# Performance work log

Measured on AMD Instinct MI355X. Metric: run time of the kernel, lower is better.

The kernel has to match this reference:

```python
import jax, jax.numpy as jnp
import numpy as np

B, T, D = 8, 2048, 1024
NUM_HEADS = 16
SCALE = 1.0 / np.sqrt(D // NUM_HEADS).astype(np.float32)  # sqrt(d_modal//num_heads), per source


def setup_inputs() -> dict:
    key = jax.random.key(0)
    ks = jax.random.split(key, 7)
    s = 1.0 / np.sqrt(D).astype(np.float32)
    return {
        "x": jax.random.normal(ks[0], (B, T, D), dtype=jnp.float32),
        "Wq_w": jax.random.normal(ks[1], (D, D), dtype=jnp.float32) * s,
        "Wq_b": jax.random.normal(ks[2], (D,), dtype=jnp.float32) * 0.01,
        "Wk_w": jax.random.normal(ks[3], (D, D), dtype=jnp.float32) * s,
        "Wk_b": jax.random.normal(ks[4], (D,), dtype=jnp.float32) * 0.01,
        "Wv_w": jax.random.normal(ks[5], (D, D), dtype=jnp.float32) * s,
        "Wv_b": jax.random.normal(ks[6], (D,), dtype=jnp.float32) * 0.01,
    }


def reference(x, Wq_w, Wq_b, Wk_w, Wk_b, Wv_w, Wv_b):
    # Linear projections (torch nn.Linear: y = x @ W.T + b)
    Q = jnp.einsum('btd,ed->bte', x, Wq_w) + Wq_b
    K = jnp.einsum('btd,ed->bte', x, Wk_w) + Wk_b
    V = jnp.einsum('btd,ed->bte', x, Wv_w) + Wv_b
    # scores [B, T, T], scaled by 1/sqrt(d_modal // num_heads) as in source
    scores = jnp.einsum('bqd,bkd->bqk', Q, K) * SCALE
    causal = jnp.tril(jnp.ones((T, T), dtype=bool))  # tril mask buffer
    scores = jnp.where(causal, scores, -jnp.inf)
    attn = jax.nn.softmax(scores, axis=-1)
    return jnp.einsum('bqk,bkd->bqd', attn, V)
```

## Files before the change

kernel.cpp:

```cpp
#include <hip/hip_runtime.h>


typedef float f32x4 __attribute__((ext_vector_type(4)));
typedef _Float16 half8 __attribute__((ext_vector_type(8)));
typedef _Float16 half4 __attribute__((ext_vector_type(4)));

#define DEVINL __device__ __forceinline__
static constexpr float ATT_SCALE = 0.125f;

DEVINL void gload_lds16(const _Float16* g, _Float16* l) {
  __builtin_amdgcn_global_load_lds((const __attribute__((address_space(1))) void*)g,
                                   (__attribute__((address_space(3))) void*)l, 16, 0, 0);
}

#define SBAR() __builtin_amdgcn_sched_barrier(0)

template <int LDA, int LDB, class GA, class GB>
DEVINL void gemm_2ph(GA ga, GB gb, int NT, char* ldsb, int tid, f32x4 acc[8][4]) {
  const int l = tid & 63, w = tid >> 6;
  const int wm = w >> 2, wn = w & 3;
  const int lr = l & 15, lk = l >> 4;
  int srow[2], scol[2];
#pragma unroll
  for (int i = 0; i < 2; ++i) {
    const int P = i * 512 + w * 64 + l;
    srow[i] = P >> 3;
    scol[i] = (P & 7) ^ (srow[i] & 7);
  }
  const int ch0 = ((lk ^ (lr & 7)) << 4);
  const int ch1 = (((lk + 4) ^ (lr & 7)) << 4);
  const int abase = lr * 128;
  const int bbase = (wn >> 1) * 16384 + (wn & 1) * 8192 + lr * 128;

  auto STGA = [&](int t, int bufb) {
#pragma unroll
    for (int h = 0; h < 2; ++h) {
      const _Float16* g0 = ga(t, h);
      char* dst = ldsb + bufb * 65536 + h * 16384;
#pragma unroll
      for (int i = 0; i < 2; ++i)
        gload_lds16(g0 + (size_t)srow[i] * LDA + scol[i] * 8,
                    (_Float16*)(dst + i * 8192 + w * 1024));
    }
  };
  auto STGB = [&](int t, int bufb) {
#pragma unroll
    for (int h = 0; h < 2; ++h) {
      const _Float16* g0 = gb(t, h);
      char* dst = ldsb + bufb * 65536 + 32768 + h * 16384;
#pragma unroll
      for (int i = 0; i < 2; ++i)
        gload_lds16(g0 + (size_t)srow[i] * LDB + scol[i] * 8,
                    (_Float16*)(dst + i * 8192 + w * 1024));
    }
  };
  half8 aA[4][2], aB[4][2], bC[4][2];
  auto RDA = [&](int bufb, int ih, half8 d[4][2]) {
    const char* sA = ldsb + bufb * 65536 + wm * 16384 + ih * 8192;
#pragma unroll
    for (int i = 0; i < 4; ++i) {
      d[i][0] = *(const half8*)(sA + abase + i * 2048 + ch0);
      d[i][1] = *(const half8*)(sA + abase + i * 2048 + ch1);
    }
  };
  auto RDB8 = [&](int bufb) {
    const char* sB = ldsb + bufb * 65536 + 32768;
#pragma unroll
    for (int j = 0; j < 4; ++j) {
      bC[j][0] = *(const half8*)(sB + bbase + j * 2048 + ch0);
      bC[j][1] = *(const half8*)(sB + bbase + j * 2048 + ch1);
    }
  };

#define MMQ() _Pragma("unroll") for (int kk_ = 0; kk_ < 2; ++kk_) \
    _Pragma("unroll") for (int i_ = 0; i_ < 4; ++i_) \
    _Pragma("unroll") for (int j_ = 0; j_ < 4; ++j_) \
      acc[i_][j_] = __builtin_amdgcn_mfma_f32_16x16x32_f16( \
          aA[i_][kk_], bC[j_][kk_], acc[i_][j_], 0, 0, 0);
#define MMH(JO) _Pragma("unroll") for (int kk_ = 0; kk_ < 2; ++kk_) \
    _Pragma("unroll") for (int i_ = 0; i_ < 4; ++i_) \
    _Pragma("unroll") for (int jj_ = 0; jj_ < 2; ++jj_) \
      acc[4 + i_][(JO) + jj_] = __builtin_amdgcn_mfma_f32_16x16x32_f16( \
          aB[i_][kk_], bC[(JO) + jj_][kk_], acc[4 + i_][(JO) + jj_], 0, 0, 0);

  STGA(0, 0); STGB(0, 0); STGB(1, 1);
  asm volatile("s_waitcnt vmcnt(4)" ::: "memory");
  __builtin_amdgcn_s_barrier(); SBAR();
  RDA(0, 0, aA);

  for (int t = 0; t < NT; ++t) {
    const int bufb = t & 1, obuf = bufb ^ 1;
    RDB8(bufb);
    RDA(bufb, 1, aB);
    if (t + 1 < NT) STGA(t + 1, obuf);
    SBAR(); __builtin_amdgcn_s_barrier();
    __builtin_amdgcn_s_setprio(1);
    MMQ();
    __builtin_amdgcn_s_setprio(0); SBAR();
    if (t + 2 < NT) {
      STGB(t + 2, bufb);
      asm volatile("s_waitcnt vmcnt(4)" ::: "memory");
    } else {
      asm volatile("s_waitcnt vmcnt(0)" ::: "memory");
    }
    SBAR(); __builtin_amdgcn_s_barrier();
    __builtin_amdgcn_s_setprio(1);
    MMH(0);
    MMH(2);
    __builtin_amdgcn_s_setprio(0);
    if (t + 1 < NT) RDA(obuf, 0, aA);
    SBAR();
  }
#undef MMQ
#undef MMH
}

template <int LDA, int LDB, class GA, class GB>
DEVINL void gemm_n128(GA ga, GB gb, int NT, char* ldsb, int tid, f32x4 acc[4][4]) {
  const int l = tid & 63, w = tid >> 6;
  const int wm = w >> 1, wn = w & 1;
  const int lr = l & 15, lk = l >> 4;
  int srow[2], scol[2];
#pragma unroll
  for (int i = 0; i < 2; ++i) {
    const int P = i * 512 + w * 64 + l;
    srow[i] = P >> 3;
    scol[i] = (P & 7) ^ (srow[i] & 7);
  }
  const int ch0 = ((lk ^ (lr & 7)) << 4);
  const int ch1 = (((lk + 4) ^ (lr & 7)) << 4);
  const int abase = (wm >> 1) * 16384 + ((wm & 1) * 64 + lr) * 128;
  const int bbase = 32768 + (wn * 64 + lr) * 128;

  auto STG = [&](const _Float16* g0, int ld, int bufb, int slot) {
    char* dst = ldsb + bufb * 49152 + slot * 16384;
#pragma unroll
    for (int i = 0; i < 2; ++i)
      gload_lds16(g0 + (size_t)srow[i] * ld + scol[i] * 8,
                  (_Float16*)(dst + i * 8192 + w * 1024));
  };
  half8 a[4][2], bfr[4][2];
  auto RD = [&](int bufb) {
    const char* bb = ldsb + bufb * 49152;
#pragma unroll
    for (int i = 0; i < 4; ++i) {
      a[i][0] = *(const half8*)(bb + abase + i * 2048 + ch0);
      a[i][1] = *(const half8*)(bb + abase + i * 2048 + ch1);
    }
#pragma unroll
    for (int j = 0; j < 4; ++j) {
      bfr[j][0] = *(const half8*)(bb + bbase + j * 2048 + ch0);
      bfr[j][1] = *(const half8*)(bb + bbase + j * 2048 + ch1);
    }
  };

  STG(ga(0, 0), LDA, 0, 0); STG(ga(0, 1), LDA, 0, 1); STG(gb(0), LDB, 0, 2);
  STG(ga(1, 0), LDA, 1, 0); STG(ga(1, 1), LDA, 1, 1); STG(gb(1), LDB, 1, 2);
  asm volatile("s_waitcnt vmcnt(6)" ::: "memory");
  __builtin_amdgcn_s_barrier();

  for (int t = 0; t < NT; ++t) {
    const int bufb = t & 1;
    RD(bufb);
    SBAR();
    __builtin_amdgcn_s_barrier();
    asm volatile("s_waitcnt lgkmcnt(0)" ::: "memory");
    SBAR();
    __builtin_amdgcn_s_setprio(1);
#pragma unroll
    for (int i = 0; i < 4; ++i)
#pragma unroll
      for (int j = 0; j < 4; ++j)
        acc[i][j] = __builtin_amdgcn_mfma_f32_16x16x32_f16(a[i][0], bfr[j][0], acc[i][j], 0, 0, 0);
    __builtin_amdgcn_s_setprio(0);
    SBAR();
    __builtin_amdgcn_s_barrier();
    if (t + 2 < NT) {
      STG(ga(t + 2, 0), LDA, bufb, 0);
      STG(ga(t + 2, 1), LDA, bufb, 1);
      STG(gb(t + 2), LDB, bufb, 2);
      asm volatile("s_waitcnt vmcnt(6)" ::: "memory");
    } else if (t + 1 < NT) {
      asm volatile("s_waitcnt vmcnt(0)" ::: "memory");
    }
    SBAR();
    __builtin_amdgcn_s_barrier();
    __builtin_amdgcn_s_setprio(1);
#pragma unroll
    for (int i = 0; i < 4; ++i)
#pragma unroll
      for (int j = 0; j < 4; ++j)
        acc[i][j] = __builtin_amdgcn_mfma_f32_16x16x32_f16(a[i][1], bfr[j][1], acc[i][j], 0, 0, 0);
    __builtin_amdgcn_s_setprio(0);
    SBAR();
    __builtin_amdgcn_s_barrier();
  }
}

__global__ __launch_bounds__(256) void cvt_all(const float* __restrict__ x,
                                               const float* __restrict__ wq,
                                               const float* __restrict__ wk,
                                               const float* __restrict__ wv,
                                               _Float16* __restrict__ xh,
                                               _Float16* __restrict__ wqh,
                                               _Float16* __restrict__ wkh,
                                               _Float16* __restrict__ wvh) {
  const int n8 = 2490368;
  for (int i = blockIdx.x * 256 + threadIdx.x; i < n8; i += 2048 * 256) {
    const float* src; _Float16* dst; int off;
    if (i < 2097152)      { src = x;  dst = xh;  off = i; }
    else if (i < 2228224) { src = wq; dst = wqh; off = i - 2097152; }
    else if (i < 2359296) { src = wk; dst = wkh; off = i - 2228224; }
    else                  { src = wv; dst = wvh; off = i - 2359296; }
    const float4* p = (const float4*)src + (size_t)off * 2;
    float4 v0 = p[0], v1 = p[1];
    half8 h;
    h[0] = (_Float16)v0.x; h[1] = (_Float16)v0.y; h[2] = (_Float16)v0.z; h[3] = (_Float16)v0.w;
    h[4] = (_Float16)v1.x; h[5] = (_Float16)v1.y; h[6] = (_Float16)v1.z; h[7] = (_Float16)v1.w;
    *((half8*)dst + off) = h;
  }
}

__global__ __launch_bounds__(512) void gemm_qkv(
    const _Float16* __restrict__ xh, const _Float16* __restrict__ Wqh,
    const _Float16* __restrict__ Wkh, const _Float16* __restrict__ Wvh,
    const float* __restrict__ bq, const float* __restrict__ bk,
    const float* __restrict__ bv, _Float16* __restrict__ Qh,
    _Float16* __restrict__ Kh, _Float16* __restrict__ VT) {
  __shared__ _Float16 lds[65536];
  const int tid = threadIdx.x;
  const int bid = blockIdx.x;
  const int swz = (bid & 7) * 96 + (bid >> 3);
  const int mt = swz / 12, nt = swz % 12;
  const int sel = nt >> 2;
  const _Float16* Wsel = sel == 0 ? Wqh : (sel == 1 ? Wkh : Wvh);
  const float* bsel = sel == 0 ? bq : (sel == 1 ? bk : bv);
  const _Float16* Ab = xh + (size_t)mt * 256 * 1024;
  const _Float16* Bb = Wsel + (size_t)(nt & 3) * 256 * 1024;
  f32x4 acc[8][4] = {};
  auto ga = [&](int t, int h) { return Ab + (size_t)h * 128 * 1024 + t * 64; };
  auto gb = [&](int t, int h) { return Bb + (size_t)h * 128 * 1024 + t * 64; };
  gemm_2ph<1024, 1024>(ga, gb, 16, (char*)lds, tid, acc);
  const int l = tid & 63, w = tid >> 6;
  const int wm = w >> 2, wn = w & 3;
  const int lr = l & 15, lk = l >> 4;
  const int n0 = (nt & 3) * 256;
  __syncthreads();
#pragma unroll
  for (int ai = 0; ai < 8; ++ai) {
    const int rbase = wm * 128 + (ai >> 2) * 64 + (ai & 3) * 16 + lk * 4;
#pragma unroll
    for (int j = 0; j < 4; ++j) {
      const int col = wn * 64 + j * 16 + lr;
      const float bvv = bsel[n0 + col];
#pragma unroll
      for (int r = 0; r < 4; ++r) {
        const int row = rbase + r;
        const float v = acc[ai][j][r] + bvv;
        if (sel < 2)
          lds[row * 256 + ((col + (row >> 2) * 16) & 255)] = (_Float16)v;
        else
          lds[col * 256 + ((row + (col >> 2) * 16) & 255)] = (_Float16)v;
      }
    }
  }
  __syncthreads();
#pragma unroll
  for (int i = 0; i < 16; ++i) {
    const int c = i * 512 + tid;
    const int row = c >> 5, c8 = c & 31;
    half8 v = *(const half8*)&lds[row * 256 + ((c8 * 8 + (row >> 2) * 16) & 255)];
    if (sel < 2) {
      _Float16* Out = sel == 0 ? Qh : Kh;
      *(half8*)&Out[(size_t)(mt * 256 + row) * 1024 + n0 + c8 * 8] = v;
    } else {
      const int bb = mt >> 3, t0 = (mt & 7) * 256;
      *(half8*)&VT[((size_t)bb * 1024 + n0 + row) * 2048 + t0 + c8 * 8] = v;
    }
  }
}

__global__ __launch_bounds__(512) void gemm_qk(const _Float16* __restrict__ Qh,
                                               const _Float16* __restrict__ Kh,
                                               _Float16* __restrict__ Sc) {
  __shared__ _Float16 lds[49152];
  const int tid = threadIdx.x;
  const int j = blockIdx.x;
  const int b = j / 72, r = j % 72;
  int qt = 0, cum = 0;
  while (cum + (qt + 1) * 2 <= r) { cum += (qt + 1) * 2; ++qt; }
  const int jn = r - cum;
  const _Float16* Ab = Qh + ((size_t)b * 2048 + qt * 256) * 1024;
  const _Float16* Bb = Kh + ((size_t)b * 2048 + jn * 128) * 1024;
  f32x4 acc[4][4] = {};
  auto ga = [&](int t, int h) { return Ab + (size_t)h * 128 * 1024 + t * 64; };
  auto gb = [&](int t) { return Bb + t * 64; };
  gemm_n128<1024, 1024>(ga, gb, 16, (char*)lds, tid, acc);
  const int l = tid & 63, w = tid >> 6;
  const int wm = w >> 1, wn = w & 1;
  const int lr = l & 15, lk = l >> 4;
  _Float16* St = Sc + ((size_t)b * 36 + (size_t)(qt * (qt + 1) / 2) + (jn >> 1)) * 65536 +
                 (jn & 1) * 128;
  const _Float16 NINF = (_Float16)(-__builtin_inff());
#pragma unroll
  for (int i = 0; i < 4; ++i) {
#pragma unroll
    for (int jj = 0; jj < 4; ++jj) {
      const int col = wn * 64 + jj * 16 + lr;
      const int kg = jn * 128 + col;
#pragma unroll
      for (int rr = 0; rr < 4; ++rr) {
        const int row = wm * 64 + i * 16 + lk * 4 + rr;
        const int qg = qt * 256 + row;
        St[(size_t)row * 256 + col] =
            (kg <= qg) ? (_Float16)(acc[i][jj][rr] * ATT_SCALE) : NINF;
      }
    }
  }
}

__global__ __launch_bounds__(256) void softmax_p(const _Float16* __restrict__ Sc,
                                                 _Float16* __restrict__ Pc) {
  const int l = threadIdx.x & 63;
  const int gid = blockIdx.x * 4 + (threadIdx.x >> 6);
  const int b = gid >> 11, q = gid & 2047;
  const int qt = q >> 8, rq = q & 255;
  const int ntile = qt + 1;
  const size_t base = ((size_t)b * 36 + (size_t)(qt * (qt + 1) / 2)) * 65536 +
                      (size_t)rq * 256 + l * 4;
  float vx[32];
  float m = -__builtin_inff();
#pragma unroll
  for (int c = 0; c < 8; ++c) {
    float x0 = -__builtin_inff(), x1 = x0, x2 = x0, x3 = x0;
    if (c < ntile) {
      half4 t = *(const half4*)&Sc[base + (size_t)c * 65536];
      x0 = (float)t[0]; x1 = (float)t[1]; x2 = (float)t[2]; x3 = (float)t[3];
    }
    vx[4 * c] = x0; vx[4 * c + 1] = x1; vx[4 * c + 2] = x2; vx[4 * c + 3] = x3;
    m = fmaxf(m, fmaxf(fmaxf(x0, x1), fmaxf(x2, x3)));
  }
#pragma unroll
  for (int s = 1; s < 64; s <<= 1) m = fmaxf(m, __shfl_xor(m, s, 64));
  float sum = 0.f;
#pragma unroll
  for (int i = 0; i < 32; ++i) { vx[i] = __expf(vx[i] - m); sum += vx[i]; }
#pragma unroll
  for (int s = 1; s < 64; s <<= 1) sum += __shfl_xor(sum, s, 64);
  const float inv = 1.f / sum;
  _Float16* Pb = Pc + base;
#pragma unroll
  for (int c = 0; c < 8; ++c) {
    if (c < ntile) {
      half4 p;
      p[0] = (_Float16)(vx[4 * c] * inv);
      p[1] = (_Float16)(vx[4 * c + 1] * inv);
      p[2] = (_Float16)(vx[4 * c + 2] * inv);
      p[3] = (_Float16)(vx[4 * c + 3] * inv);
      *(half4*)&Pb[(size_t)c * 65536] = p;
    }
  }
}

__global__ __launch_bounds__(512) void gemm_pv(const _Float16* __restrict__ Pc,
                                               const _Float16* __restrict__ VT,
                                               float* __restrict__ O) {
  __shared__ _Float16 lds[49152];
  const int tid = threadIdx.x;
  const int j = blockIdx.x;
  const int qt = 7 - (j >> 6);
  const int dt = (j >> 3) & 7, b = j & 7;
  const _Float16* Pb = Pc + ((size_t)b * 36 + (size_t)(qt * (qt + 1) / 2)) * 65536;
  const _Float16* Vb = VT + ((size_t)b * 1024 + dt * 128) * 2048;
  f32x4 acc[4][4] = {};
  auto ga = [&](int t, int h) {
    return Pb + (size_t)(t >> 2) * 65536 + (size_t)h * 32768 + (t & 3) * 64;
  };
  auto gb = [&](int t) { return Vb + t * 64; };
  gemm_n128<256, 2048>(ga, gb, (qt + 1) * 4, (char*)lds, tid, acc);
  const int l = tid & 63, w = tid >> 6;
  const int wm = w >> 1, wn = w & 1;
  const int lr = l & 15, lk = l >> 4;
#pragma unroll
  for (int i = 0; i < 4; ++i) {
#pragma unroll
    for (int jj = 0; jj < 4; ++jj) {
      const int cg = dt * 128 + wn * 64 + jj * 16 + lr;
#pragma unroll
      for (int rr = 0; rr < 4; ++rr) {
        const int rg = qt * 256 + wm * 64 + i * 16 + lk * 4 + rr;
        O[((size_t)b * 2048 + rg) * 1024 + cg] = acc[i][jj][rr];
      }
    }
  }
}

extern "C" void kernel_launch(void* const* d_in, const int* in_sizes, int n_in,
                              void* d_out, int out_size, void* d_ws, size_t ws_size,
                              hipStream_t stream) {
  const float* x    = (const float*)d_in[0];
  const float* Wq_w = (const float*)d_in[1];
  const float* Wq_b = (const float*)d_in[2];
  const float* Wk_w = (const float*)d_in[3];
  const float* Wk_b = (const float*)d_in[4];
  const float* Wv_w = (const float*)d_in[5];
  const float* Wv_b = (const float*)d_in[6];
  float* out = (float*)d_out;
  char* ws = (char*)d_ws;
  _Float16* xh  = (_Float16*)(ws);
  _Float16* Wqh = (_Float16*)(ws + 33554432);
  _Float16* Wkh = (_Float16*)(ws + 35651584);
  _Float16* Wvh = (_Float16*)(ws + 37748736);
  _Float16* Sc  = (_Float16*)(ws);
  _Float16* Qh  = (_Float16*)(ws + 75497472);
  _Float16* Kh  = (_Float16*)(ws + 109051904);
  _Float16* Pc  = (_Float16*)(ws + 75497472);
  _Float16* VT  = (_Float16*)(ws + 142606336);

  cvt_all<<<2048, 256, 0, stream>>>(x, Wq_w, Wk_w, Wv_w, xh, Wqh, Wkh, Wvh);
  gemm_qkv<<<768, 512, 0, stream>>>(xh, Wqh, Wkh, Wvh, Wq_b, Wk_b, Wv_b, Qh, Kh, VT);
  gemm_qk<<<576, 512, 0, stream>>>(Qh, Kh, Sc);
  softmax_p<<<4096, 256, 0, stream>>>(Sc, Pc);
  gemm_pv<<<512, 512, 0, stream>>>(Pc, VT, out);
}
```

Before: 274.0 us.

## Unify GEMMs into 256-thread 256x128 tiles with K=32 steps and smaller LDS

```diff
diff --git a/kernel.cpp b/kernel.cpp
--- a/kernel.cpp
+++ b/kernel.cpp
@@ -16,182 +16,73 @@
 #define SBAR() __builtin_amdgcn_sched_barrier(0)
 
 template <int LDA, int LDB, class GA, class GB>
-DEVINL void gemm_2ph(GA ga, GB gb, int NT, char* ldsb, int tid, f32x4 acc[8][4]) {
-  const int l = tid & 63, w = tid >> 6;
-  const int wm = w >> 2, wn = w & 3;
-  const int lr = l & 15, lk = l >> 4;
-  int srow[2], scol[2];
-#pragma unroll
-  for (int i = 0; i < 2; ++i) {
-    const int P = i * 512 + w * 64 + l;
-    srow[i] = P >> 3;
-    scol[i] = (P & 7) ^ (srow[i] & 7);
-  }
-  const int ch0 = ((lk ^ (lr & 7)) << 4);
-  const int ch1 = (((lk + 4) ^ (lr & 7)) << 4);
-  const int abase = lr * 128;
-  const int bbase = (wn >> 1) * 16384 + (wn & 1) * 8192 + lr * 128;
-
-  auto STGA = [&](int t, int bufb) {
-#pragma unroll
-    for (int h = 0; h < 2; ++h) {
-      const _Float16* g0 = ga(t, h);
-      char* dst = ldsb + bufb * 65536 + h * 16384;
-#pragma unroll
-      for (int i = 0; i < 2; ++i)
-        gload_lds16(g0 + (size_t)srow[i] * LDA + scol[i] * 8,
-                    (_Float16*)(dst + i * 8192 + w * 1024));
-    }
-  };
-  auto STGB = [&](int t, int bufb) {
-#pragma unroll
-    for (int h = 0; h < 2; ++h) {
-      const _Float16* g0 = gb(t, h);
-      char* dst = ldsb + bufb * 65536 + 32768 + h * 16384;
-#pragma unroll
-      for (int i = 0; i < 2; ++i)
-        gload_lds16(g0 + (size_t)srow[i] * LDB + scol[i] * 8,
-                    (_Float16*)(dst + i * 8192 + w * 1024));
-    }
-  };
-  half8 aA[4][2], aB[4][2], bC[4][2];
-  auto RDA = [&](int bufb, int ih, half8 d[4][2]) {
-    const char* sA = ldsb + bufb * 65536 + wm * 16384 + ih * 8192;
-#pragma unroll
-    for (int i = 0; i < 4; ++i) {
-      d[i][0] = *(const half8*)(sA + abase + i * 2048 + ch0);
-      d[i][1] = *(const half8*)(sA + abase + i * 2048 + ch1);
-    }
-  };
-  auto RDB8 = [&](int bufb) {
-    const char* sB = ldsb + bufb * 65536 + 32768;
-#pragma unroll
-    for (int j = 0; j < 4; ++j) {
-      bC[j][0] = *(const half8*)(sB + bbase + j * 2048 + ch0);
-      bC[j][1] = *(const half8*)(sB + bbase + j * 2048 + ch1);
-    }
-  };
-
-#define MMQ() _Pragma("unroll") for (int kk_ = 0; kk_ < 2; ++kk_) \
-    _Pragma("unroll") for (int i_ = 0; i_ < 4; ++i_) \
-    _Pragma("unroll") for (int j_ = 0; j_ < 4; ++j_) \
-      acc[i_][j_] = __builtin_amdgcn_mfma_f32_16x16x32_f16( \
-          aA[i_][kk_], bC[j_][kk_], acc[i_][j_], 0, 0, 0);
-#define MMH(JO) _Pragma("unroll") for (int kk_ = 0; kk_ < 2; ++kk_) \
-    _Pragma("unroll") for (int i_ = 0; i_ < 4; ++i_) \
-    _Pragma("unroll") for (int jj_ = 0; jj_ < 2; ++jj_) \
-      acc[4 + i_][(JO) + jj_] = __builtin_amdgcn_mfma_f32_16x16x32_f16( \
-          aB[i_][kk_], bC[(JO) + jj_][kk_], acc[4 + i_][(JO) + jj_], 0, 0, 0);
-
-  STGA(0, 0); STGB(0, 0); STGB(1, 1);
-  asm volatile("s_waitcnt vmcnt(4)" ::: "memory");
-  __builtin_amdgcn_s_barrier(); SBAR();
-  RDA(0, 0, aA);
-
-  for (int t = 0; t < NT; ++t) {
-    const int bufb = t & 1, obuf = bufb ^ 1;
-    RDB8(bufb);
-    RDA(bufb, 1, aB);
-    if (t + 1 < NT) STGA(t + 1, obuf);
-    SBAR(); __builtin_amdgcn_s_barrier();
-    __builtin_amdgcn_s_setprio(1);
-    MMQ();
-    __builtin_amdgcn_s_setprio(0); SBAR();
-    if (t + 2 < NT) {
-      STGB(t + 2, bufb);
-      asm volatile("s_waitcnt vmcnt(4)" ::: "memory");
-    } else {
-      asm volatile("s_waitcnt vmcnt(0)" ::: "memory");
-    }
-    SBAR(); __builtin_amdgcn_s_barrier();
-    __builtin_amdgcn_s_setprio(1);
-    MMH(0);
-    MMH(2);
-    __builtin_amdgcn_s_setprio(0);
-    if (t + 1 < NT) RDA(obuf, 0, aA);
-    SBAR();
-  }
-#undef MMQ
-#undef MMH
-}
-
-template <int LDA, int LDB, class GA, class GB>
-DEVINL void gemm_n128(GA ga, GB gb, int NT, char* ldsb, int tid, f32x4 acc[4][4]) {
+DEVINL void gemm_mb(GA ga, GB gb, int NT, char* ldsb, int tid, f32x4 acc[8][4]) {
   const int l = tid & 63, w = tid >> 6;
   const int wm = w >> 1, wn = w & 1;
   const int lr = l & 15, lk = l >> 4;
-  int srow[2], scol[2];
+  int arow[4], acol[4], brow[2], bcol[2];
+#pragma unroll
+  for (int i = 0; i < 4; ++i) {
+    const int P = i * 256 + tid;
+    arow[i] = P >> 2;
+    acol[i] = (P & 3) ^ ((arow[i] >> 1) & 3);
+  }
 #pragma unroll
   for (int i = 0; i < 2; ++i) {
-    const int P = i * 512 + w * 64 + l;
-    srow[i] = P >> 3;
-    scol[i] = (P & 7) ^ (srow[i] & 7);
-  }
-  const int ch0 = ((lk ^ (lr & 7)) << 4);
-  const int ch1 = (((lk + 4) ^ (lr & 7)) << 4);
-  const int abase = (wm >> 1) * 16384 + ((wm & 1) * 64 + lr) * 128;
-  const int bbase = 32768 + (wn * 64 + lr) * 128;
-
-  auto STG = [&](const _Float16* g0, int ld, int bufb, int slot) {
-    char* dst = ldsb + bufb * 49152 + slot * 16384;
+    const int P = i * 256 + tid;
+    brow[i] = P >> 2;
+    bcol[i] = (P & 3) ^ ((brow[i] >> 1) & 3);
+  }
+  int aoff[8], boff[4];
+#pragma unroll
+  for (int i = 0; i < 8; ++i) {
+    const int r = wm * 128 + i * 16 + lr;
+    aoff[i] = r * 64 + ((lk ^ ((r >> 1) & 3)) << 4);
+  }
+#pragma unroll
+  for (int j = 0; j < 4; ++j) {
+    const int r = wn * 64 + j * 16 + lr;
+    boff[j] = 16384 + r * 64 + ((lk ^ ((r >> 1) & 3)) << 4);
+  }
+  auto STG = [&](int t, int bufoff) {
+    const _Float16* gA = ga(t);
+#pragma unroll
+    for (int i = 0; i < 4; ++i)
+      gload_lds16(gA + (size_t)arow[i] * LDA + acol[i] * 8,
+                  (_Float16*)(ldsb + bufoff + i * 4096 + w * 1024));
+    const _Float16* gB = gb(t);
 #pragma unroll
     for (int i = 0; i < 2; ++i)
-      gload_lds16(g0 + (size_t)srow[i] * ld + scol[i] * 8,
-                  (_Float16*)(dst + i * 8192 + w * 1024));
+      gload_lds16(gB + (size_t)brow[i] * LDB + bcol[i] * 8,
+                  (_Float16*)(ldsb + bufoff + 16384 + i * 4096 + w * 1024));
   };
-  half8 a[4][2], bfr[4][2];
-  auto RD = [&](int bufb) {
-    const char* bb = ldsb + bufb * 49152;
-#pragma unroll
-    for (int i = 0; i < 4; ++i) {
-      a[i][0] = *(const half8*)(bb + abase + i * 2048 + ch0);
-      a[i][1] = *(const half8*)(bb + abase + i * 2048 + ch1);
-    }
-#pragma unroll
-    for (int j = 0; j < 4; ++j) {
-      bfr[j][0] = *(const half8*)(bb + bbase + j * 2048 + ch0);
-      bfr[j][1] = *(const half8*)(bb + bbase + j * 2048 + ch1);
-    }
-  };
-
-  STG(ga(0, 0), LDA, 0, 0); STG(ga(0, 1), LDA, 0, 1); STG(gb(0), LDB, 0, 2);
-  STG(ga(1, 0), LDA, 1, 0); STG(ga(1, 1), LDA, 1, 1); STG(gb(1), LDB, 1, 2);
+
+  STG(0, 0);
+  STG(1, 24576);
   asm volatile("s_waitcnt vmcnt(6)" ::: "memory");
   __builtin_amdgcn_s_barrier();
 
+  half8 a[8], b[4];
   for (int t = 0; t < NT; ++t) {
-    const int bufb = t & 1;
-    RD(bufb);
+    const int bufoff = (t & 1) * 24576;
+    const char* bb = ldsb + bufoff;
+#pragma unroll
+    for (int i = 0; i < 8; ++i) a[i] = *(const half8*)(bb + aoff[i]);
+#pragma unroll
+    for (int j = 0; j < 4; ++j) b[j] = *(const half8*)(bb + boff[j]);
+    asm volatile("s_waitcnt lgkmcnt(0)" ::: "memory");
     SBAR();
     __builtin_amdgcn_s_barrier();
-    asm volatile("s_waitcnt lgkmcnt(0)" ::: "memory");
-    SBAR();
+    if (t + 2 < NT) STG(t + 2, bufoff);
     __builtin_amdgcn_s_setprio(1);
 #pragma unroll
-    for (int i = 0; i < 4; ++i)
+    for (int i = 0; i < 8; ++i)
 #pragma unroll
       for (int j = 0; j < 4; ++j)
-        acc[i][j] = __builtin_amdgcn_mfma_f32_16x16x32_f16(a[i][0], bfr[j][0], acc[i][j], 0, 0, 0);
+        acc[i][j] = __builtin_amdgcn_mfma_f32_16x16x32_f16(a[i], b[j], acc[i][j], 0, 0, 0);
     __builtin_amdgcn_s_setprio(0);
-    SBAR();
-    __builtin_amdgcn_s_barrier();
-    if (t + 2 < NT) {
-      STG(ga(t + 2, 0), LDA, bufb, 0);
-      STG(ga(t + 2, 1), LDA, bufb, 1);
-      STG(gb(t + 2), LDB, bufb, 2);
-      asm volatile("s_waitcnt vmcnt(6)" ::: "memory");
-    } else if (t + 1 < NT) {
-      asm volatile("s_waitcnt vmcnt(0)" ::: "memory");
-    }
-    SBAR();
-    __builtin_amdgcn_s_barrier();
-    __builtin_amdgcn_s_setprio(1);
-#pragma unroll
-    for (int i = 0; i < 4; ++i)
-#pragma unroll
-      for (int j = 0; j < 4; ++j)
-        acc[i][j] = __builtin_amdgcn_mfma_f32_16x16x32_f16(a[i][1], bfr[j][1], acc[i][j], 0, 0, 0);
-    __builtin_amdgcn_s_setprio(0);
+    if (t + 2 < NT) { asm volatile("s_waitcnt vmcnt(6)" ::: "memory"); }
+    else            { asm volatile("s_waitcnt vmcnt(0)" ::: "memory"); }
     SBAR();
     __builtin_amdgcn_s_barrier();
   }
@@ -221,69 +112,98 @@
   }
 }
 
-__global__ __launch_bounds__(512) void gemm_qkv(
+__global__ __launch_bounds__(256, 3) void gemm_qkv(
     const _Float16* __restrict__ xh, const _Float16* __restrict__ Wqh,
     const _Float16* __restrict__ Wkh, const _Float16* __restrict__ Wvh,
     const float* __restrict__ bq, const float* __restrict__ bk,
     const float* __restrict__ bv, _Float16* __restrict__ Qh,
     _Float16* __restrict__ Kh, _Float16* __restrict__ VT) {
-  __shared__ _Float16 lds[65536];
+  __shared__ _Float16 lds[24576];
   const int tid = threadIdx.x;
   const int bid = blockIdx.x;
-  const int swz = (bid & 7) * 96 + (bid >> 3);
-  const int mt = swz / 12, nt = swz % 12;
-  const int sel = nt >> 2;
+  const int swz = (bid & 7) * 192 + (bid >> 3);
+  const int mt = swz / 24, nt = swz % 24;
+  const int sel = nt >> 3;
   const _Float16* Wsel = sel == 0 ? Wqh : (sel == 1 ? Wkh : Wvh);
   const float* bsel = sel == 0 ? bq : (sel == 1 ? bk : bv);
+  const int n0 = (nt & 7) * 128;
   const _Float16* Ab = xh + (size_t)mt * 256 * 1024;
-  const _Float16* Bb = Wsel + (size_t)(nt & 3) * 256 * 1024;
+  const _Float16* Bb = Wsel + (size_t)n0 * 1024;
   f32x4 acc[8][4] = {};
-  auto ga = [&](int t, int h) { return Ab + (size_t)h * 128 * 1024 + t * 64; };
-  auto gb = [&](int t, int h) { return Bb + (size_t)h * 128 * 1024 + t * 64; };
-  gemm_2ph<1024, 1024>(ga, gb, 16, (char*)lds, tid, acc);
+  auto ga = [&](int t) { return Ab + t * 32; };
+  auto gb = [&](int t) { return Bb + t * 32; };
+  gemm_mb<1024, 1024>(ga, gb, 32, (char*)lds, tid, acc);
   const int l = tid & 63, w = tid >> 6;
-  const int wm = w >> 2, wn = w & 3;
+  const int wm = w >> 1, wn = w & 1;
   const int lr = l & 15, lk = l >> 4;
-  const int n0 = (nt & 3) * 256;
   __syncthreads();
-#pragma unroll
-  for (int ai = 0; ai < 8; ++ai) {
-    const int rbase = wm * 128 + (ai >> 2) * 64 + (ai & 3) * 16 + lk * 4;
-#pragma unroll
-    for (int j = 0; j < 4; ++j) {
-      const int col = wn * 64 + j * 16 + lr;
-      const float bvv = bsel[n0 + col];
-#pragma unroll
-      for (int r = 0; r < 4; ++r) {
-        const int row = rbase + r;
-        const float v = acc[ai][j][r] + bvv;
-        if (sel < 2)
-          lds[row * 256 + ((col + (row >> 2) * 16) & 255)] = (_Float16)v;
-        else
-          lds[col * 256 + ((row + (col >> 2) * 16) & 255)] = (_Float16)v;
-      }
-    }
-  }
-  __syncthreads();
-#pragma unroll
-  for (int i = 0; i < 16; ++i) {
-    const int c = i * 512 + tid;
-    const int row = c >> 5, c8 = c & 31;
-    half8 v = *(const half8*)&lds[row * 256 + ((c8 * 8 + (row >> 2) * 16) & 255)];
-    if (sel < 2) {
-      _Float16* Out = sel == 0 ? Qh : Kh;
-      *(half8*)&Out[(size_t)(mt * 256 + row) * 1024 + n0 + c8 * 8] = v;
-    } else {
-      const int bb = mt >> 3, t0 = (mt & 7) * 256;
-      *(half8*)&VT[((size_t)bb * 1024 + n0 + row) * 2048 + t0 + c8 * 8] = v;
-    }
-  }
-}
-
-__global__ __launch_bounds__(512) void gemm_qk(const _Float16* __restrict__ Qh,
-                                               const _Float16* __restrict__ Kh,
-                                               _Float16* __restrict__ Sc) {
-  __shared__ _Float16 lds[49152];
+  if (sel < 2) {
+    _Float16* Out = sel == 0 ? Qh : Kh;
+#pragma unroll
+    for (int h = 0; h < 2; ++h) {
+      if (wm == h) {
+#pragma unroll
+        for (int ai = 0; ai < 8; ++ai) {
+#pragma unroll
+          for (int j = 0; j < 4; ++j) {
+            const int col = wn * 64 + j * 16 + lr;
+            const float bvv = bsel[n0 + col];
+#pragma unroll
+            for (int r = 0; r < 4; ++r) {
+              const int rl = ai * 16 + lk * 4 + r;
+              lds[rl * 128 + ((col + (rl >> 2) * 8) & 127)] =
+                  (_Float16)(acc[ai][j][r] + bvv);
+            }
+          }
+        }
+      }
+      __syncthreads();
+#pragma unroll
+      for (int i = 0; i < 8; ++i) {
+        const int c = i * 256 + tid;
+        const int rl = c >> 4, c8 = c & 15;
+        half8 v = *(const half8*)&lds[rl * 128 + ((c8 * 8 + (rl >> 2) * 8) & 127)];
+        *(half8*)&Out[(size_t)(mt * 256 + h * 128 + rl) * 1024 + n0 + c8 * 8] = v;
+      }
+      __syncthreads();
+    }
+  } else {
+    const int bb = mt >> 3, t0 = (mt & 7) * 256;
+#pragma unroll
+    for (int h = 0; h < 2; ++h) {
+      if (wn == h) {
+#pragma unroll
+        for (int ai = 0; ai < 8; ++ai) {
+#pragma unroll
+          for (int j = 0; j < 4; ++j) {
+            const int cl = j * 16 + lr;
+            const float bvv = bsel[n0 + h * 64 + cl];
+#pragma unroll
+            for (int r = 0; r < 4; ++r) {
+              const int row = wm * 128 + ai * 16 + lk * 4 + r;
+              lds[cl * 256 + ((row + (cl >> 2) * 8) & 255)] =
+                  (_Float16)(acc[ai][j][r] + bvv);
+            }
+          }
+        }
+      }
+      __syncthreads();
+#pragma unroll
+      for (int i = 0; i < 8; ++i) {
+        const int c = i * 256 + tid;
+        const int d = c >> 5, t8 = c & 31;
+        half8 v = *(const half8*)&lds[d * 256 + ((t8 * 8 + (d >> 2) * 8) & 255)];
+        *(half8*)&VT[((size_t)bb * 1024 + n0 + h * 64 + d) * 2048 + t0 + t8 * 8] = v;
+      }
+      __syncthreads();
+    }
+  }
+}
+
+__global__ __launch_bounds__(256, 3) void gemm_qk(const _Float16* __restrict__ Qh,
+                                                  const _Float16* __restrict__ Kh,
+                                                  _Float16* __restrict__ Sc) {
+  __shared__ _Float16 lds[24576];
   const int tid = threadIdx.x;
   const int j = blockIdx.x;
   const int b = j / 72, r = j % 72;
@@ -292,10 +212,10 @@
   const int jn = r - cum;
   const _Float16* Ab = Qh + ((size_t)b * 2048 + qt * 256) * 1024;
   const _Float16* Bb = Kh + ((size_t)b * 2048 + jn * 128) * 1024;
-  f32x4 acc[4][4] = {};
-  auto ga = [&](int t, int h) { return Ab + (size_t)h * 128 * 1024 + t * 64; };
-  auto gb = [&](int t) { return Bb + t * 64; };
-  gemm_n128<1024, 1024>(ga, gb, 16, (char*)lds, tid, acc);
+  f32x4 acc[8][4] = {};
+  auto ga = [&](int t) { return Ab + t * 32; };
+  auto gb = [&](int t) { return Bb + t * 32; };
+  gemm_mb<1024, 1024>(ga, gb, 32, (char*)lds, tid, acc);
   const int l = tid & 63, w = tid >> 6;
   const int wm = w >> 1, wn = w & 1;
   const int lr = l & 15, lk = l >> 4;
@@ -303,17 +223,17 @@
                  (jn & 1) * 128;
   const _Float16 NINF = (_Float16)(-__builtin_inff());
 #pragma unroll
-  for (int i = 0; i < 4; ++i) {
+  for (int ai = 0; ai < 8; ++ai) {
 #pragma unroll
     for (int jj = 0; jj < 4; ++jj) {
       const int col = wn * 64 + jj * 16 + lr;
       const int kg = jn * 128 + col;
 #pragma unroll
       for (int rr = 0; rr < 4; ++rr) {
-        const int row = wm * 64 + i * 16 + lk * 4 + rr;
+        const int row = wm * 128 + ai * 16 + lk * 4 + rr;
         const int qg = qt * 256 + row;
         St[(size_t)row * 256 + col] =
-            (kg <= qg) ? (_Float16)(acc[i][jj][rr] * ATT_SCALE) : NINF;
+            (kg <= qg) ? (_Float16)(acc[ai][jj][rr] * ATT_SCALE) : NINF;
       }
     }
   }
@@ -362,34 +282,32 @@
   }
 }
 
-__global__ __launch_bounds__(512) void gemm_pv(const _Float16* __restrict__ Pc,
-                                               const _Float16* __restrict__ VT,
-                                               float* __restrict__ O) {
-  __shared__ _Float16 lds[49152];
+__global__ __launch_bounds__(256, 3) void gemm_pv(const _Float16* __restrict__ Pc,
+                                                  const _Float16* __restrict__ VT,
+                                                  float* __restrict__ O) {
+  __shared__ _Float16 lds[24576];
   const int tid = threadIdx.x;
   const int j = blockIdx.x;
   const int qt = 7 - (j >> 6);
   const int dt = (j >> 3) & 7, b = j & 7;
   const _Float16* Pb = Pc + ((size_t)b * 36 + (size_t)(qt * (qt + 1) / 2)) * 65536;
   const _Float16* Vb = VT + ((size_t)b * 1024 + dt * 128) * 2048;
-  f32x4 acc[4][4] = {};
-  auto ga = [&](int t, int h) {
-    return Pb + (size_t)(t >> 2) * 65536 + (size_t)h * 32768 + (t & 3) * 64;
-  };
-  auto gb = [&](int t) { return Vb + t * 64; };
-  gemm_n128<256, 2048>(ga, gb, (qt + 1) * 4, (char*)lds, tid, acc);
+  f32x4 acc[8][4] = {};
+  auto ga = [&](int t) { return Pb + (size_t)(t >> 3) * 65536 + (t & 7) * 32; };
+  auto gb = [&](int t) { return Vb + t * 32; };
+  gemm_mb<256, 2048>(ga, gb, (qt + 1) * 8, (char*)lds, tid, acc);
   const int l = tid & 63, w = tid >> 6;
   const int wm = w >> 1, wn = w & 1;
   const int lr = l & 15, lk = l >> 4;
 #pragma unroll
-  for (int i = 0; i < 4; ++i) {
+  for (int ai = 0; ai < 8; ++ai) {
 #pragma unroll
     for (int jj = 0; jj < 4; ++jj) {
       const int cg = dt * 128 + wn * 64 + jj * 16 + lr;
 #pragma unroll
       for (int rr = 0; rr < 4; ++rr) {
-        const int rg = qt * 256 + wm * 64 + i * 16 + lk * 4 + rr;
-        O[((size_t)b * 2048 + rg) * 1024 + cg] = acc[i][jj][rr];
+        const int rg = qt * 256 + wm * 128 + ai * 16 + lk * 4 + rr;
+        O[((size_t)b * 2048 + rg) * 1024 + cg] = acc[ai][jj][rr];
       }
     }
   }
@@ -418,8 +336,8 @@
   _Float16* VT  = (_Float16*)(ws + 142606336);
 
   cvt_all<<<2048, 256, 0, stream>>>(x, Wq_w, Wk_w, Wv_w, xh, Wqh, Wkh, Wvh);
-  gemm_qkv<<<768, 512, 0, stream>>>(xh, Wqh, Wkh, Wvh, Wq_b, Wk_b, Wv_b, Qh, Kh, VT);
-  gemm_qk<<<576, 512, 0, stream>>>(Qh, Kh, Sc);
+  gemm_qkv<<<1536, 256, 0, stream>>>(xh, Wqh, Wkh, Wvh, Wq_b, Wk_b, Wv_b, Qh, Kh, VT);
+  gemm_qk<<<576, 256, 0, stream>>>(Qh, Kh, Sc);
   softmax_p<<<4096, 256, 0, stream>>>(Sc, Pc);
-  gemm_pv<<<512, 512, 0, stream>>>(Pc, VT, out);
-}
+  gemm_pv<<<512, 256, 0, stream>>>(Pc, VT, out);
+}
```

Result: slower. 908.2 us (+231.4%).
